# Kernel tuning notes

Measured on AMD Instinct MI355X. Metric: run time of the kernel, lower is better.

The kernel has to match this reference:

```python
import jax, jax.numpy as jnp
import numpy as np

NC = 1      # constants.nc (Game-of-Life grid channels)
GRID = 32
PAD_ITERS = 31


def _iterated_wrap_idx(n, p):
    # Faithfully simulate p iterations of circular pad-1 on a growing axis.
    # NOTE: this is NOT a single wrap-pad of p; the border alternates 0/n-1.
    idx = np.arange(n)
    for _ in range(p):
        idx = np.concatenate([idx[-1:], idx, idx[:1]])
    return jnp.asarray(idx)

_IDX = _iterated_wrap_idx(GRID, PAD_ITERS)  # length 94, static


def _pad(x):
    # one gather per spatial dim replaces the 31-iteration concat loop
    return x[:, :, _IDX][:, :, :, _IDX]


def _conv(x, w, b, stride):
    y = jax.lax.conv_general_dilated(
        x, w, window_strides=(stride, stride), padding='VALID',
        dimension_numbers=('NCHW', 'OIHW', 'NCHW'))
    return y + b[None, :, None, None]


def setup_inputs() -> dict:
    key = jax.random.key(0)
    ks = jax.random.split(key, 7)
    B = 16
    s_in = 1.0 / np.sqrt(NC * 32 * 32)      # fan-in init, keeps activations sane
    s_hid = 1.0 / np.sqrt(32 * 32 * 32)
    s_out = 1.0 / np.sqrt(32)
    return {
        'x': jax.random.normal(ks[0], (B, NC, GRID, GRID), jnp.float32),
        'in_w': jax.random.normal(ks[1], (32, NC, 32, 32), jnp.float32) * s_in,
        'in_b': jnp.zeros((32,), jnp.float32),
        'convs_w': jax.random.normal(ks[2], (20, 32, 32, 32, 32), jnp.float32) * s_hid,
        'convs_b': jnp.zeros((20, 32), jnp.float32),
        'out_w': jax.random.normal(ks[3], (NC, 32, 1, 1), jnp.float32) * s_out,
        'out_b': jnp.zeros((NC,), jnp.float32),
    }


def reference(x, in_w, in_b, convs_w, convs_b, out_w, out_b):
    # in_conv: pad(31 iters) + conv k=32 s=2 (no ReLU, as in original)
    h = _conv(_pad(x), in_w, in_b, 2)           # [B,32,32,32]

    def step(h, wb):
        w, b = wb
        h = jax.nn.relu(_conv(_pad(h), w, b, 2))
        return h, None

    h, _ = jax.lax.scan(step, h, (convs_w, convs_b))  # 20 hidden layers
    return _conv(h, out_w, out_b, 1)             # 1x1 out conv, no activation
```

## Files before the change

### kernel.cpp

```cpp
#include <hip/hip_runtime.h>


typedef _Float16 f16;
typedef _Float16 f16x8 __attribute__((ext_vector_type(8)));
typedef float f32x4 __attribute__((ext_vector_type(4)));
typedef float f32x16 __attribute__((ext_vector_type(16)));

__device__ __forceinline__ int mwrap(int j) {
  int t = j - 31;
  if ((unsigned)t <= 31u) return t;
  if (t < 0) return (j & 1) ? 0 : 31;
  return (j & 1) ? 0 : 31;
}


template <int CIN, bool RELU, bool PRE>
__global__ __launch_bounds__(512, 2) void gemm3(
    const void* __restrict__ Wv,
    const f16* __restrict__ hp_in,
    const float* __restrict__ bias,
    f16* __restrict__ hp_out) {
  __shared__ __align__(16) f16 rowbuf[2][32][96];
  __shared__ float Red[8][2][1024];

  const int tid = threadIdx.x;
  const int lane = tid & 63;
  const int w = tid >> 6;
  const int ox = lane & 31;
  const int s = lane >> 5;

  const int pair0 = blockIdx.x * 2;
  const int b = pair0 >> 5;
  const int oy0 = pair0 & 31;

  const int rrow = tid / 12, rseg = tid - rrow * 12;

  int ybase[6];
#pragma unroll
  for (int j = 0; j < 6; ++j) ybase[j] = mwrap(2 * oy0 + 4 * w + j);

  f32x16 acc0 = {}, acc1 = {};
  f16x8 A0[8], A1[8];
  f16x8 stg = {};

  auto loadA = [&](int c, f16x8* dst) {
#pragma unroll
    for (int kyi = 0; kyi < 4; ++kyi) {
#pragma unroll
      for (int kxh = 0; kxh < 2; ++kxh) {
        const int ky = 4 * w + kyi;
        const int chunk = (c * 32 + ky) * 2 + kxh;
        if constexpr (PRE) {
          const f16* Wl = (const f16*)Wv;
          dst[kyi * 2 + kxh] = *(const f16x8*)(Wl + (size_t)chunk * 512 + lane * 8);
        } else {
          const float* Wl = (const float*)Wv;
          const float* sp = Wl + (((size_t)(ox * CIN + c) * 32 + ky) * 32 + kxh * 16 + s * 8);
          f32x4 u0 = *(const f32x4*)sp;
          f32x4 u1 = *(const f32x4*)(sp + 4);
          f16x8 v;
          v[0] = (f16)u0[0]; v[1] = (f16)u0[1]; v[2] = (f16)u0[2]; v[3] = (f16)u0[3];
          v[4] = (f16)u1[0]; v[5] = (f16)u1[1]; v[6] = (f16)u1[2]; v[7] = (f16)u1[3];
          dst[kyi * 2 + kxh] = v;
        }
      }
    }
  };
  auto loadRow = [&](int c) {
    if (tid < 384)
      stg = *(const f16x8*)(hp_in + ((size_t)(b * CIN + c) * 32 + rrow) * 96 + rseg * 8);
  };
  auto writeRow = [&](int nb) {
    if (tid < 384) *(f16x8*)(&rowbuf[nb][rrow][rseg * 8]) = stg;
  };

  auto body = [&](int c, const f16x8* Ause, f16x8* Apre) {
    const int buf = c & 1;
    const bool pre = (c + 1 < CIN);
    if (pre) {
      loadRow(c + 1);
      __builtin_amdgcn_sched_barrier(0);
      loadA(c + 1, Apre);
    }
    f16x8 F[6][2];
#pragma unroll
    for (int j = 0; j < 6; ++j) {
      const int* R = (const int*)(&rowbuf[buf][ybase[j]][0]);
#pragma unroll
      for (int kxh = 0; kxh < 2; ++kxh) {
        const int bi = ox + 4 * s + 8 * kxh;
        int4 t;
        t.x = R[bi]; t.y = R[bi + 1]; t.z = R[bi + 2]; t.w = R[bi + 3];
        F[j][kxh] = __builtin_bit_cast(f16x8, t);
      }
    }
#pragma unroll
    for (int kyi = 0; kyi < 4; ++kyi) {
#pragma unroll
      for (int kxh = 0; kxh < 2; ++kxh) {
        const f16x8 a = Ause[kyi * 2 + kxh];
        acc0 = __builtin_amdgcn_mfma_f32_32x32x16_f16(a, F[kyi][kxh], acc0, 0, 0, 0);
        acc1 = __builtin_amdgcn_mfma_f32_32x32x16_f16(a, F[kyi + 2][kxh], acc1, 0, 0, 0);
      }
    }
    if (pre) writeRow(buf ^ 1);
    asm volatile("s_waitcnt lgkmcnt(0)" ::: "memory");
    __builtin_amdgcn_sched_barrier(0);
    __builtin_amdgcn_s_barrier();
  };

  loadA(0, A0);
  loadRow(0);
  writeRow(0);
  __syncthreads();

  if constexpr (CIN == 1) {
    body(0, A0, A1);
  } else {
#pragma unroll 1
    for (int c = 0; c < CIN; c += 2) {
      body(c, A0, A1);
      body(c + 1, A1, A0);
    }
  }

#pragma unroll
  for (int r = 0; r < 16; ++r) {
    Red[w][0][r * 64 + lane] = acc0[r];
    Red[w][1][r * 64 + lane] = acc1[r];
  }
  __syncthreads();

#pragma unroll
  for (int k4 = 0; k4 < 4; ++k4) {
    const int o = tid + 512 * k4;
    const int p = o >> 10, co = (o >> 5) & 31, oxx = o & 31;
    const int idx = ((co & 3) + 4 * (co >> 3)) * 64 + ((co >> 2) & 1) * 32 + oxx;
    float v = bias[co];
#pragma unroll
    for (int w8 = 0; w8 < 8; ++w8) v += Red[w8][p][idx];
    if (RELU) v = fmaxf(v, 0.f);
    const f16 hv = (f16)v;
    f16* base = hp_out + ((size_t)(b * 32 + co) * 32 + (oy0 + p)) * 96;
    base[oxx + 31] = hv;
    if (oxx == 0) {
#pragma unroll
      for (int j = 1; j <= 29; j += 2) base[j] = hv;
#pragma unroll
      for (int j = 63; j <= 93; j += 2) base[j] = hv;
    }
    if (oxx == 31) {
#pragma unroll
      for (int j = 0; j <= 30; j += 2) base[j] = hv;
#pragma unroll
      for (int j = 64; j <= 92; j += 2) base[j] = hv;
    }
  }
}

__global__ void pad_x_kernel(const float* __restrict__ x, f16* __restrict__ xp) {
  const int i = blockIdx.x * 256 + threadIdx.x;
  if (i >= 48128) return;
  const int bq = i / 3008, r = i - bq * 3008;
  const int y = r / 94, j = r - y * 94;
  xp[bq * 3072 + y * 96 + j] = (f16)x[(bq * 32 + y) * 32 + mwrap(j)];
}

__global__ void convert_w3(const float* __restrict__ in_w,
                           const float* __restrict__ convs_w,
                           f16* __restrict__ WfIn, f16* __restrict__ WfH) {
  const int total = 4096 + 20 * 131072;
  for (int g = blockIdx.x * blockDim.x + threadIdx.x; g < total;
       g += gridDim.x * blockDim.x) {
    const float* src;
    f16* dst;
    int chunk, lanE, c, ky, kxh;
    if (g < 4096) {
      chunk = g >> 6; lanE = g & 63;
      kxh = chunk & 1; ky = chunk >> 1; c = 0;
      const int co = lanE & 31, ss = lanE >> 5;
      src = in_w + ((size_t)(co * 1 + 0) * 32 + ky) * 32 + kxh * 16 + ss * 8;
      dst = WfIn + (size_t)chunk * 512 + lanE * 8;
    } else {
      const int h = g - 4096;
      const int layer = h >> 17, r = h & 131071;
      chunk = r >> 6; lanE = r & 63;
      kxh = chunk & 1;
      const int t = chunk >> 1;
      ky = t & 31; c = t >> 5;
      const int co = lanE & 31, ss = lanE >> 5;
      src = convs_w + (size_t)layer * 1048576 +
            ((size_t)(co * 32 + c) * 32 + ky) * 32 + kxh * 16 + ss * 8;
      dst = WfH + (size_t)layer * 1048576 + (size_t)chunk * 512 + lanE * 8;
    }
    f32x4 u0 = *(const f32x4*)src;
    f32x4 u1 = *(const f32x4*)(src + 4);
    f16x8 v;
    v[0] = (f16)u0[0]; v[1] = (f16)u0[1]; v[2] = (f16)u0[2]; v[3] = (f16)u0[3];
    v[4] = (f16)u1[0]; v[5] = (f16)u1[1]; v[6] = (f16)u1[2]; v[7] = (f16)u1[3];
    *(f16x8*)dst = v;
  }
}

__global__ void out_conv3(const f16* __restrict__ hp,
                          const float* __restrict__ ow,
                          const float* __restrict__ ob,
                          float* __restrict__ out) {
  const int o = blockIdx.x * 256 + threadIdx.x;
  const int b = o >> 10, oy = (o >> 5) & 31, oxx = o & 31;
  float s = ob[0];
#pragma unroll
  for (int c = 0; c < 32; ++c)
    s += ow[c] * (float)hp[((size_t)(b * 32 + c) * 32 + oy) * 96 + oxx + 31];
  out[o] = s;
}

extern "C" void kernel_launch(void* const* d_in, const int* in_sizes, int n_in,
                              void* d_out, int out_size, void* d_ws,
                              size_t ws_size, hipStream_t stream) {
  const float* x = (const float*)d_in[0];
  const float* in_w = (const float*)d_in[1];
  const float* in_b = (const float*)d_in[2];
  const float* convs_w = (const float*)d_in[3];
  const float* convs_b = (const float*)d_in[4];
  const float* out_w = (const float*)d_in[5];
  const float* out_b = (const float*)d_in[6];
  float* out = (float*)d_out;

  char* ws = (char*)d_ws;
  f16* xpad = (f16*)ws;
  f16* hpA = (f16*)(ws + 98304);
  f16* hpB = (f16*)(ws + 98304 + 3145728);
  f16* WfIn = (f16*)(ws + 6389760);
  f16* WfH = (f16*)(ws + 6455296);
  const bool pre = (ws_size >= 48398336ull);

  pad_x_kernel<<<188, 256, 0, stream>>>(x, xpad);
  if (pre) convert_w3<<<2048, 256, 0, stream>>>(in_w, convs_w, WfIn, WfH);

  if (pre)
    gemm3<1, false, true><<<256, 512, 0, stream>>>(WfIn, xpad, in_b, hpA);
  else
    gemm3<1, false, false><<<256, 512, 0, stream>>>(in_w, xpad, in_b, hpA);

  for (int l = 0; l < 20; ++l) {
    const f16* cur = (l % 2 == 0) ? hpA : hpB;
    f16* nxt = (l % 2 == 0) ? hpB : hpA;
    if (pre)
      gemm3<32, true, true><<<256, 512, 0, stream>>>(
          WfH + (size_t)l * 1048576, cur, convs_b + 32 * l, nxt);
    else
      gemm3<32, true, false><<<256, 512, 0, stream>>>(
          convs_w + (size_t)l * 1048576, cur, convs_b + 32 * l, nxt);
  }

  out_conv3<<<64, 256, 0, stream>>>(hpA, out_w, out_b, out);
}
```

Baseline: 978.6 us.

## Double the row buffers and process channels in pairs to halve barriers

The input-row shared buffer grows from 2 to 4 slots, and the channel loop now handles 4 channels per iteration, staging two rows at a time. A block barrier is taken only once per 2 channels instead of every channel. LDS row pointers are precomputed per slot so address arithmetic leaves the inner loop. This cuts synchronisation overhead and lengthens overlap of global loads with MFMA work, at the cost of more LDS and more live registers (two staging vectors plus pointer arrays), which could hurt occupancy under the 512x2 launch bounds.

```diff
diff --git a/kernel.cpp b/kernel.cpp
--- a/kernel.cpp
+++ b/kernel.cpp
@@ -13,6 +13,37 @@
   return (j & 1) ? 0 : 31;
 }
 
+
+#define GOLBODY(PB, AUSE)                                                   \
+  {                                                                         \
+    f16x8 F[6][2];                                                          \
+    _Pragma("unroll")                                                       \
+    for (int j_ = 0; j_ < 6; ++j_) {                                        \
+      int4 t0_, t1_;                                                        \
+      t0_.x = PB[j_][0]; t0_.y = PB[j_][1];                                 \
+      t0_.z = PB[j_][2]; t0_.w = PB[j_][3];                                 \
+      t1_.x = PB[j_][8]; t1_.y = PB[j_][9];                                 \
+      t1_.z = PB[j_][10]; t1_.w = PB[j_][11];                               \
+      F[j_][0] = __builtin_bit_cast(f16x8, t0_);                            \
+      F[j_][1] = __builtin_bit_cast(f16x8, t1_);                            \
+    }                                                                       \
+    _Pragma("unroll")                                                       \
+    for (int kyi_ = 0; kyi_ < 4; ++kyi_) {                                  \
+      _Pragma("unroll")                                                     \
+      for (int kxh_ = 0; kxh_ < 2; ++kxh_) {                                \
+        const f16x8 a_ = AUSE[kyi_ * 2 + kxh_];                             \
+        acc0 = __builtin_amdgcn_mfma_f32_32x32x16_f16(a_, F[kyi_][kxh_],    \
+                                                      acc0, 0, 0, 0);       \
+        acc1 = __builtin_amdgcn_mfma_f32_32x32x16_f16(a_, F[kyi_ + 2][kxh_],\
+                                                      acc1, 0, 0, 0);       \
+      }                                                                     \
+    }                                                                       \
+  }
+
+#define GOLBAR()                                       \
+  asm volatile("s_waitcnt lgkmcnt(0)" ::: "memory");   \
+  __builtin_amdgcn_sched_barrier(0);                   \
+  __builtin_amdgcn_s_barrier();
 
 template <int CIN, bool RELU, bool PRE>
 __global__ __launch_bounds__(512, 2) void gemm3(
@@ -20,7 +51,7 @@
     const f16* __restrict__ hp_in,
     const float* __restrict__ bias,
     f16* __restrict__ hp_out) {
-  __shared__ __align__(16) f16 rowbuf[2][32][96];
+  __shared__ __align__(16) f16 rowbuf[4][32][96];
   __shared__ float Red[8][2][1024];
 
   const int tid = threadIdx.x;
@@ -39,9 +70,19 @@
 #pragma unroll
   for (int j = 0; j < 6; ++j) ybase[j] = mwrap(2 * oy0 + 4 * w + j);
 
+  const int bi = ox + 4 * s;
+  const int *P0[6], *P1[6], *P2[6], *P3[6];
+#pragma unroll
+  for (int j = 0; j < 6; ++j) {
+    P0[j] = (const int*)(&rowbuf[0][ybase[j]][0]) + bi;
+    P1[j] = (const int*)(&rowbuf[1][ybase[j]][0]) + bi;
+    P2[j] = (const int*)(&rowbuf[2][ybase[j]][0]) + bi;
+    P3[j] = (const int*)(&rowbuf[3][ybase[j]][0]) + bi;
+  }
+
   f32x16 acc0 = {}, acc1 = {};
   f16x8 A0[8], A1[8];
-  f16x8 stg = {};
+  f16x8 stgA = {}, stgB = {};
 
   auto loadA = [&](int c, f16x8* dst) {
 #pragma unroll
@@ -66,61 +107,55 @@
       }
     }
   };
-  auto loadRow = [&](int c) {
+  auto loadRowTo = [&](int c, f16x8& dst) {
     if (tid < 384)
-      stg = *(const f16x8*)(hp_in + ((size_t)(b * CIN + c) * 32 + rrow) * 96 + rseg * 8);
+      dst = *(const f16x8*)(hp_in + ((size_t)(b * CIN + c) * 32 + rrow) * 96 + rseg * 8);
   };
-  auto writeRow = [&](int nb) {
-    if (tid < 384) *(f16x8*)(&rowbuf[nb][rrow][rseg * 8]) = stg;
+  auto writeRow = [&](int nb, const f16x8& src) {
+    if (tid < 384) *(f16x8*)(&rowbuf[nb][rrow][rseg * 8]) = src;
   };
 
-  auto body = [&](int c, const f16x8* Ause, f16x8* Apre) {
-    const int buf = c & 1;
-    const bool pre = (c + 1 < CIN);
-    if (pre) {
-      loadRow(c + 1);
-      __builtin_amdgcn_sched_barrier(0);
-      loadA(c + 1, Apre);
-    }
-    f16x8 F[6][2];
-#pragma unroll
-    for (int j = 0; j < 6; ++j) {
-      const int* R = (const int*)(&rowbuf[buf][ybase[j]][0]);
-#pragma unroll
-      for (int kxh = 0; kxh < 2; ++kxh) {
-        const int bi = ox + 4 * s + 8 * kxh;
-        int4 t;
-        t.x = R[bi]; t.y = R[bi + 1]; t.z = R[bi + 2]; t.w = R[bi + 3];
-        F[j][kxh] = __builtin_bit_cast(f16x8, t);
+  if constexpr (CIN == 1) {
+    loadRowTo(0, stgA);
+    writeRow(0, stgA);
+    loadA(0, A0);
+    __syncthreads();
+    GOLBODY(P0, A0);
+  } else {
+    static_assert(CIN % 4 == 0, "CIN must be 1 or multiple of 4");
+    loadRowTo(0, stgA);
+    loadRowTo(1, stgB);
+    writeRow(0, stgA);
+    writeRow(1, stgB);
+    loadA(0, A0);
+    __syncthreads();
+
+#pragma unroll 1
+    for (int gg = 0; gg < CIN / 4; ++gg) {
+      const int c0 = 4 * gg;
+      loadRowTo(c0 + 2, stgA);
+      loadRowTo(c0 + 3, stgB);
+      loadA(c0 + 1, A1);
+      GOLBODY(P0, A0);
+      loadA(c0 + 2, A0);
+      GOLBODY(P1, A1);
+      writeRow(2, stgA);
+      writeRow(3, stgB);
+      GOLBAR();
+      const bool more = (c0 + 4 < CIN);
+      if (more) {
+        loadRowTo(c0 + 4, stgA);
+        loadRowTo(c0 + 5, stgB);
       }
-    }
-#pragma unroll
-    for (int kyi = 0; kyi < 4; ++kyi) {
-#pragma unroll
-      for (int kxh = 0; kxh < 2; ++kxh) {
-        const f16x8 a = Ause[kyi * 2 + kxh];
-        acc0 = __builtin_amdgcn_mfma_f32_32x32x16_f16(a, F[kyi][kxh], acc0, 0, 0, 0);
-        acc1 = __builtin_amdgcn_mfma_f32_32x32x16_f16(a, F[kyi + 2][kxh], acc1, 0, 0, 0);
+      loadA(c0 + 3, A1);
+      GOLBODY(P2, A0);
+      if (more) loadA(c0 + 4, A0);
+      GOLBODY(P3, A1);
+      if (more) {
+        writeRow(0, stgA);
+        writeRow(1, stgB);
+        GOLBAR();
       }
-    }
-    if (pre) writeRow(buf ^ 1);
-    asm volatile("s_waitcnt lgkmcnt(0)" ::: "memory");
-    __builtin_amdgcn_sched_barrier(0);
-    __builtin_amdgcn_s_barrier();
-  };
-
-  loadA(0, A0);
-  loadRow(0);
-  writeRow(0);
-  __syncthreads();
-
-  if constexpr (CIN == 1) {
-    body(0, A0, A1);
-  } else {
-#pragma unroll 1
-    for (int c = 0; c < CIN; c += 2) {
-      body(c, A0, A1);
-      body(c + 1, A1, A0);
     }
   }
 
```

Measured after the change: 948.2 us. -3.1%, faster.

## Load conv input rows directly from global memory into registers, dropping LDS staging

Applied to the files above, without the earlier changes.

Removes the shared-memory row buffer and per-channel block barriers. Each lane now reads its 6x2 input fragments straight from the padded global activation through cached, 4-byte-aligned vector loads, and the next channel's fragments and weights are double-buffered in registers. This is meant to cut the LDS write/read and the s_barrier that each input channel paid for. In exchange it issues more, unaligned global loads with redundancy across waves and uses more registers, which may hurt occupancy.

```diff
diff --git a/kernel.cpp b/kernel.cpp
--- a/kernel.cpp
+++ b/kernel.cpp
@@ -5,6 +5,7 @@
 typedef _Float16 f16x8 __attribute__((ext_vector_type(8)));
 typedef float f32x4 __attribute__((ext_vector_type(4)));
 typedef float f32x16 __attribute__((ext_vector_type(16)));
+typedef int i4a __attribute__((ext_vector_type(4), aligned(4)));
 
 __device__ __forceinline__ int mwrap(int j) {
   int t = j - 31;
@@ -13,6 +14,21 @@
   return (j & 1) ? 0 : 31;
 }
 
+
+#define MFMAC(AUSE, FD)                                                      \
+  {                                                                          \
+    _Pragma("unroll")                                                        \
+    for (int kyi_ = 0; kyi_ < 4; ++kyi_) {                                   \
+      _Pragma("unroll")                                                      \
+      for (int kxh_ = 0; kxh_ < 2; ++kxh_) {                                 \
+        const f16x8 a_ = AUSE[kyi_ * 2 + kxh_];                              \
+        acc0 = __builtin_amdgcn_mfma_f32_32x32x16_f16(a_, FD[kyi_][kxh_],    \
+                                                      acc0, 0, 0, 0);        \
+        acc1 = __builtin_amdgcn_mfma_f32_32x32x16_f16(a_, FD[kyi_ + 2][kxh_],\
+                                                      acc1, 0, 0, 0);        \
+      }                                                                      \
+    }                                                                        \
+  }
 
 template <int CIN, bool RELU, bool PRE>
 __global__ __launch_bounds__(512, 2) void gemm3(
@@ -20,7 +36,6 @@
     const f16* __restrict__ hp_in,
     const float* __restrict__ bias,
     f16* __restrict__ hp_out) {
-  __shared__ __align__(16) f16 rowbuf[2][32][96];
   __shared__ float Red[8][2][1024];
 
   const int tid = threadIdx.x;
@@ -33,15 +48,16 @@
   const int b = pair0 >> 5;
   const int oy0 = pair0 & 31;
 
-  const int rrow = tid / 12, rseg = tid - rrow * 12;
-
-  int ybase[6];
-#pragma unroll
-  for (int j = 0; j < 6; ++j) ybase[j] = mwrap(2 * oy0 + 4 * w + j);
+  const int bi = ox + 4 * s;
+  const int* Rb[6];
+#pragma unroll
+  for (int j = 0; j < 6; ++j)
+    Rb[j] = (const int*)hp_in +
+            ((size_t)b * CIN * 32 + mwrap(2 * oy0 + 4 * w + j)) * 48 + bi;
 
   f32x16 acc0 = {}, acc1 = {};
   f16x8 A0[8], A1[8];
-  f16x8 stg = {};
+  f16x8 F0[6][2], F1[6][2];
 
   auto loadA = [&](int c, f16x8* dst) {
 #pragma unroll
@@ -66,64 +82,38 @@
       }
     }
   };
-  auto loadRow = [&](int c) {
-    if (tid < 384)
-      stg = *(const f16x8*)(hp_in + ((size_t)(b * CIN + c) * 32 + rrow) * 96 + rseg * 8);
+  auto loadF = [&](int c, f16x8 (*FD)[2]) {
+    const int coff = c * 48 * 32;
+#pragma unroll
+    for (int j = 0; j < 6; ++j) {
+      const int* R = Rb[j] + coff;
+      FD[j][0] = __builtin_bit_cast(f16x8, *(const i4a*)(R));
+      FD[j][1] = __builtin_bit_cast(f16x8, *(const i4a*)(R + 8));
+    }
   };
-  auto writeRow = [&](int nb) {
-    if (tid < 384) *(f16x8*)(&rowbuf[nb][rrow][rseg * 8]) = stg;
-  };
-
-  auto body = [&](int c, const f16x8* Ause, f16x8* Apre) {
-    const int buf = c & 1;
-    const bool pre = (c + 1 < CIN);
-    if (pre) {
-      loadRow(c + 1);
-      __builtin_amdgcn_sched_barrier(0);
-      loadA(c + 1, Apre);
-    }
-    f16x8 F[6][2];
-#pragma unroll
-    for (int j = 0; j < 6; ++j) {
-      const int* R = (const int*)(&rowbuf[buf][ybase[j]][0]);
-#pragma unroll
-      for (int kxh = 0; kxh < 2; ++kxh) {
-        const int bi = ox + 4 * s + 8 * kxh;
-        int4 t;
-        t.x = R[bi]; t.y = R[bi + 1]; t.z = R[bi + 2]; t.w = R[bi + 3];
-        F[j][kxh] = __builtin_bit_cast(f16x8, t);
-      }
-    }
-#pragma unroll
-    for (int kyi = 0; kyi < 4; ++kyi) {
-#pragma unroll
-      for (int kxh = 0; kxh < 2; ++kxh) {
-        const f16x8 a = Ause[kyi * 2 + kxh];
-        acc0 = __builtin_amdgcn_mfma_f32_32x32x16_f16(a, F[kyi][kxh], acc0, 0, 0, 0);
-        acc1 = __builtin_amdgcn_mfma_f32_32x32x16_f16(a, F[kyi + 2][kxh], acc1, 0, 0, 0);
-      }
-    }
-    if (pre) writeRow(buf ^ 1);
-    asm volatile("s_waitcnt lgkmcnt(0)" ::: "memory");
-    __builtin_amdgcn_sched_barrier(0);
-    __builtin_amdgcn_s_barrier();
-  };
-
-  loadA(0, A0);
-  loadRow(0);
-  writeRow(0);
-  __syncthreads();
 
   if constexpr (CIN == 1) {
-    body(0, A0, A1);
+    loadA(0, A0);
+    loadF(0, F0);
+    MFMAC(A0, F0);
   } else {
+    static_assert(CIN % 2 == 0, "CIN must be 1 or even");
+    loadA(0, A0);
+    loadF(0, F0);
 #pragma unroll 1
     for (int c = 0; c < CIN; c += 2) {
-      body(c, A0, A1);
-      body(c + 1, A1, A0);
-    }
-  }
-
+      loadA(c + 1, A1);
+      loadF(c + 1, F1);
+      MFMAC(A0, F0);
+      if (c + 2 < CIN) {
+        loadA(c + 2, A0);
+        loadF(c + 2, F0);
+      }
+      MFMAC(A1, F1);
+    }
+  }
+
+  __syncthreads();
 #pragma unroll
   for (int r = 0; r < 16; ++r) {
     Red[w][0][r * 64 + lane] = acc0[r];
```

After: 1.158 ms. 1.18x slower.
